# Kernel optimization log

Hardware: AMD Instinct MI355X
Metric: run time of the kernel (lower is better)

Reference implementation:

```python
import jax, jax.numpy as jnp
import numpy as np

B, N, C = 8, 2000, 81
MAX_INST = 100
MIN_CONF = 0.7
NMS_THR = 0.3
BBOX_STD = jnp.array([0.1, 0.1, 0.2, 0.2], dtype=jnp.float32)
CLASS_OFFSET = 4.0  # per-class box offset so one NMS == per-class NMS


def setup_inputs() -> dict:
    key = jax.random.key(0)
    k1, k2, k3, k4 = jax.random.split(key, 4)
    # well-formed normalized rois: y1<y2, x1<x2
    ctr = jax.random.uniform(k1, (B, N, 2), minval=0.2, maxval=0.8)
    sz = jax.random.uniform(k2, (B, N, 2), minval=0.02, maxval=0.3)
    y1x1 = jnp.clip(ctr - 0.5 * sz, 0.0, 1.0)
    y2x2 = jnp.clip(ctr + 0.5 * sz, 0.0, 1.0)
    rois = jnp.concatenate([y1x1, y2x2], axis=-1).astype(jnp.float32)
    mrcnn_class = jax.nn.softmax(4.0 * jax.random.normal(k3, (B, N, C)), axis=-1).astype(jnp.float32)
    mrcnn_bbox = (0.1 * jax.random.normal(k4, (B, N, C, 4))).astype(jnp.float32)
    # meta: [image_id(1), orig_shape(3), image_shape(3), window(4), scale(1), active_class_ids(C)]
    meta_row = np.concatenate([
        np.array([0.0]), np.array([1024.0, 1024.0, 3.0]), np.array([1024.0, 1024.0, 3.0]),
        np.array([0.0, 0.0, 1024.0, 1024.0]), np.array([1.0]), np.ones(C)]).astype(np.float32)
    image_meta = jnp.broadcast_to(jnp.asarray(meta_row), (B, 12 + C))
    return {"rois": rois, "mrcnn_class": mrcnn_class, "mrcnn_bbox": mrcnn_bbox, "image_meta": image_meta}


def _apply_box_deltas(boxes, deltas):  # [N,4],[N,4]
    h = boxes[:, 2] - boxes[:, 0]
    w = boxes[:, 3] - boxes[:, 1]
    cy = boxes[:, 0] + 0.5 * h + deltas[:, 0] * h
    cx = boxes[:, 1] + 0.5 * w + deltas[:, 1] * w
    h = h * jnp.exp(deltas[:, 2])
    w = w * jnp.exp(deltas[:, 3])
    return jnp.stack([cy - 0.5 * h, cx - 0.5 * w, cy + 0.5 * h, cx + 0.5 * w], axis=1)


def _clip_boxes(boxes, window):  # window: [4]
    wy1, wx1, wy2, wx2 = window[0], window[1], window[2], window[3]
    y1 = jnp.clip(boxes[:, 0], wy1, wy2)
    x1 = jnp.clip(boxes[:, 1], wx1, wx2)
    y2 = jnp.clip(boxes[:, 2], wy1, wy2)
    x2 = jnp.clip(boxes[:, 3], wx1, wx2)
    return jnp.stack([y1, x1, y2, x2], axis=1)


def _pairwise_iou(b):  # [N,4] -> [N,N]
    area = (b[:, 2] - b[:, 0]) * (b[:, 3] - b[:, 1])
    iy = jnp.maximum(0.0, jnp.minimum(b[:, None, 2], b[None, :, 2]) - jnp.maximum(b[:, None, 0], b[None, :, 0]))
    ix = jnp.maximum(0.0, jnp.minimum(b[:, None, 3], b[None, :, 3]) - jnp.maximum(b[:, None, 1], b[None, :, 1]))
    inter = iy * ix
    return inter / (area[:, None] + area[None, :] - inter + 1e-12)


def _refine_one(rois, probs, deltas, window):
    n = rois.shape[0]
    class_ids = jnp.argmax(probs, axis=1)                      # [N]
    idx = jnp.arange(n)
    scores = probs[idx, class_ids]                              # [N]
    ds = deltas[idx, class_ids] * BBOX_STD                      # [N,4]
    refined = _clip_boxes(_apply_box_deltas(rois, ds), window)  # [N,4]
    valid = (class_ids > 0) & (scores >= MIN_CONF)
    # per-class NMS via class-offset trick (classes can never overlap)
    off_boxes = refined + CLASS_OFFSET * class_ids.astype(jnp.float32)[:, None]
    order = jnp.argsort(-jnp.where(valid, scores, -1.0))
    b_sorted = off_boxes[order]
    iou = _pairwise_iou(b_sorted)                               # [N,N]
    pos = jnp.arange(n)

    def body(keep, i):
        sup = keep[i] & (iou[i] > NMS_THR) & (pos > i)
        return keep & ~sup, None

    keep_sorted, _ = jax.lax.scan(body, valid[order], pos)
    keep = jnp.zeros(n, bool).at[order].set(keep_sorted)
    # per-class cap at MAX_INST (mirror max_output_size of per-class NMS)
    same = class_ids[:, None] == class_ids[None, :]
    before = (scores[None, :] > scores[:, None]) | ((scores[None, :] == scores[:, None]) & (pos[None, :] < pos[:, None]))
    rank = jnp.sum(keep[None, :] & same & before, axis=1)
    keep = keep & (rank < MAX_INST)
    # global top-k by score, pad with zeros
    masked = jnp.where(keep, scores, -1.0)
    top_scores, top_idx = jax.lax.top_k(masked, MAX_INST)
    valid_out = top_scores > 0.0
    det = jnp.concatenate([
        refined[top_idx],
        class_ids[top_idx].astype(jnp.float32)[:, None],
        scores[top_idx][:, None]], axis=1)                      # [MAX_INST,6]
    return jnp.where(valid_out[:, None], det, 0.0)


def reference(rois, mrcnn_class, mrcnn_bbox, image_meta):
    # normalize per-image window using image_shape of first image (as in original)
    image_shape = image_meta[0, 4:7]
    h, w = image_shape[0], image_shape[1]
    scale = jnp.stack([h, w, h, w]) - 1.0
    shift = jnp.array([0.0, 0.0, 1.0, 1.0], dtype=jnp.float32)
    window = (image_meta[:, 7:11] - shift) / scale              # [B,4]
    det = jax.vmap(_refine_one)(rois, mrcnn_class, mrcnn_bbox, window)
    return det.reshape(rois.shape[0], MAX_INST, 6)
```

## Files before the change

### kernel.cpp

```cpp
#include <hip/hip_runtime.h>
#include <stdint.h>

#define Bn 8
#define Nn 2000
#define Cc 81
#define META_STRIDE (12 + Cc)
#define MAXI 100
#define MINCONF 0.7f
#define NMSTHR 0.3f
#define PB_ROIS 128
#define PSTRIDE 83
#define SELT 320
#define SELCAP 512

__device__ __forceinline__ uint32_t ford(float f) {
    uint32_t u = __float_as_uint(f);
    return (u & 0x80000000u) ? ~u : (u | 0x80000000u);
}

__device__ __forceinline__ unsigned long long shflx64(unsigned long long v, int lx) {
    unsigned int lo = (unsigned int)v, hi = (unsigned int)(v >> 32);
    lo = (unsigned int)__shfl_xor((int)lo, lx, 64);
    hi = (unsigned int)__shfl_xor((int)hi, lx, 64);
    return ((unsigned long long)hi << 32) | lo;
}

__global__ void __launch_bounds__(256)
k_prep(const float* __restrict__ rois,
       const float* __restrict__ probs,
       const float* __restrict__ bbox,
       const float* __restrict__ meta,
       float* __restrict__ refined,
       float* __restrict__ score,
       int* __restrict__ cls,
       unsigned long long* __restrict__ keys) {
    __shared__ float sp[PB_ROIS * PSTRIDE];
    int tid  = threadIdx.x;
    int base = blockIdx.x * PB_ROIS;

    const float* gp = probs + (size_t)base * Cc;
    const int total = PB_ROIS * Cc;
    int r = tid / Cc, c = tid - r * Cc;
    for (int idx = tid; idx < total; idx += 256) {
        sp[r * PSTRIDE + c] = gp[idx];
        r += 3; c += 13;
        if (c >= Cc) { c -= Cc; r += 1; }
    }
    __syncthreads();

    int row  = tid >> 1;
    int half = tid & 1;
    const float* sr = sp + row * PSTRIDE;
    int   c0 = half ? 41 : 0;
    int   c1 = half ? Cc : 41;
    float v  = sr[c0];
    int   cb = c0;
    for (int cc2 = c0 + 1; cc2 < c1; ++cc2) {
        float x = sr[cc2];
        if (x > v) { v = x; cb = cc2; }
    }
    float vo = __shfl_xor(v, 1, 64);
    int   co = __shfl_xor(cb, 1, 64);
    float vA = half ? vo : v;   int cA = half ? co : cb;
    float vB = half ? v  : vo;  int cB = half ? cb : co;
    float sbest;  int cbest;
    if (vB > vA) { sbest = vB; cbest = cB; }
    else         { sbest = vA; cbest = cA; }

    if (half) return;
    int t = base + row;

    float4 d4 = reinterpret_cast<const float4*>(bbox)[(size_t)t * Cc + cbest];
    float dy = d4.x * 0.1f, dx = d4.y * 0.1f, dh = d4.z * 0.2f, dw = d4.w * 0.2f;

    float4 r4 = reinterpret_cast<const float4*>(rois)[t];
    float y1 = r4.x, x1 = r4.y, y2 = r4.z, x2 = r4.w;
    float h = y2 - y1, w = x2 - x1;
    float cy = y1 + 0.5f * h + dy * h;
    float cx = x1 + 0.5f * w + dx * w;
    h = h * expf(dh);
    w = w * expf(dw);
    float ny1 = cy - 0.5f * h, nx1 = cx - 0.5f * w;
    float ny2 = cy + 0.5f * h, nx2 = cx + 0.5f * w;

    int b = t / Nn;
    float sy = meta[4] - 1.0f, sx = meta[5] - 1.0f;
    const float* mb = meta + (size_t)b * META_STRIDE;
    float wy1 = mb[7] / sy;
    float wx1 = mb[8] / sx;
    float wy2 = (mb[9]  - 1.0f) / sy;
    float wx2 = (mb[10] - 1.0f) / sx;

    ny1 = fminf(fmaxf(ny1, wy1), wy2);
    nx1 = fminf(fmaxf(nx1, wx1), wx2);
    ny2 = fminf(fmaxf(ny2, wy1), wy2);
    nx2 = fminf(fmaxf(nx2, wx1), wx2);

    reinterpret_cast<float4*>(refined)[t] = float4{ny1, nx1, ny2, nx2};
    score[t] = sbest;
    cls[t]   = cbest;

    int i = t - b * Nn;
    bool valid = (cbest > 0) && (sbest >= MINCONF);
    float ks = valid ? sbest : -1.0f;
    keys[t] = ((unsigned long long)ford(ks) << 32) |
              (unsigned long long)(0xFFFFFFFFu - (uint32_t)i);
}

__global__ void __launch_bounds__(1024, 1)
k_select(const unsigned long long* __restrict__ keys,
         unsigned long long* __restrict__ selk,
         int* __restrict__ selcnt) {
    __shared__ int h1[256], h2[256], sc[256];
    __shared__ int sB, sSuf, sTheta, scnt;

    int b = blockIdx.x, tid = threadIdx.x;
    const unsigned long long* kb = keys + (size_t)b * Nn;
    int e0 = tid << 1;
    unsigned long long k0 = (e0     < Nn) ? kb[e0]     : 0ull;
    unsigned long long k1 = (e0 + 1 < Nn) ? kb[e0 + 1] : 0ull;

    if (tid < 256) { h1[tid] = 0; h2[tid] = 0; }
    if (tid == 0) { sB = -2; sSuf = 0; sTheta = 0x8000; scnt = 0; }
    __syncthreads();

    if (k0 >> 63) atomicAdd(&h1[(int)(k0 >> 56) & 255], 1);
    if (k1 >> 63) atomicAdd(&h1[(int)(k1 >> 56) & 255], 1);
    __syncthreads();

    if (tid < 256) sc[tid] = h1[tid];
    __syncthreads();
    for (int off = 1; off < 256; off <<= 1) {
        int v = 0;
        if (tid < 256 && tid + off < 256) v = sc[tid + off];
        __syncthreads();
        if (tid < 256) sc[tid] += v;
        __syncthreads();
    }
    if (tid < 256) {
        int c  = sc[tid];
        int cn = (tid < 255) ? sc[tid + 1] : 0;
        if (c >= SELT && cn < SELT) { sB = tid; sSuf = cn; }
    }
    __syncthreads();
    int B = sB;

    if (B >= 0) {
        if ((k0 >> 63) && (((int)(k0 >> 56) & 255) == B))
            atomicAdd(&h2[(int)(k0 >> 48) & 255], 1);
        if ((k1 >> 63) && (((int)(k1 >> 56) & 255) == B))
            atomicAdd(&h2[(int)(k1 >> 48) & 255], 1);
        __syncthreads();
        if (tid < 256) sc[tid] = h2[tid];
        __syncthreads();
        for (int off = 1; off < 256; off <<= 1) {
            int v = 0;
            if (tid < 256 && tid + off < 256) v = sc[tid + off];
            __syncthreads();
            if (tid < 256) sc[tid] += v;
            __syncthreads();
        }
        if (tid < 256) {
            int c  = sSuf + sc[tid];
            int cn = sSuf + ((tid < 255) ? sc[tid + 1] : 0);
            if (c >= SELT && cn < SELT) sTheta = (B << 8) | tid;
        }
    }
    __syncthreads();

    unsigned th = (unsigned)sTheta;
    if ((unsigned)(k0 >> 48) >= th) {
        int s = atomicAdd(&scnt, 1);
        if (s < SELCAP) selk[b * SELCAP + s] = k0;
    }
    if ((unsigned)(k1 >> 48) >= th) {
        int s = atomicAdd(&scnt, 1);
        if (s < SELCAP) selk[b * SELCAP + s] = k1;
    }
    __syncthreads();
    if (tid == 0) { int c = scnt; selcnt[b] = c < SELCAP ? c : SELCAP; }
}

__global__ void __launch_bounds__(1024, 1)
k_rest(const unsigned long long* __restrict__ selk,
       const int* __restrict__ selcnt,
       const float* __restrict__ refined,
       const float* __restrict__ score,
       const int* __restrict__ cls,
       float* __restrict__ out) {
    __shared__ unsigned long long sk[SELCAP];
    __shared__ float4 sboxL[SELCAP];
    __shared__ unsigned long long intraw[64];
    __shared__ unsigned long long extw[16];
    __shared__ int klist[128];
    __shared__ int sNk;

    int b = blockIdx.x, tid = threadIdx.x;
    int wid = tid >> 6, lane = tid & 63;
    int e0 = tid << 1;

    int S = selcnt[b];
    if (tid < SELCAP) sk[tid] = (tid < S) ? selk[b * SELCAP + tid] : 0ull;
    if (tid == 0) sNk = 0;
    __syncthreads();

    if (tid < 256) {
        unsigned long long a = sk[e0], bv = sk[e0 + 1];
        for (int k = 2; k <= 128; k <<= 1) {
            bool desc = ((e0 & k) == 0);
            for (int j = k >> 1; j >= 2; j >>= 1) {
                int lx = j >> 1;
                bool keepmax = (desc == ((lane & lx) == 0));
                unsigned long long oa = shflx64(a, lx);
                unsigned long long ob = shflx64(bv, lx);
                a  = keepmax ? (a  > oa ? a  : oa) : (a  < oa ? a  : oa);
                bv = keepmax ? (bv > ob ? bv : ob) : (bv < ob ? bv : ob);
            }
            bool sw = desc ? (a < bv) : (a > bv);
            if (sw) { unsigned long long t2 = a; a = bv; bv = t2; }
        }
        sk[e0] = a; sk[e0 + 1] = bv;
    }
    __syncthreads();

    for (int k = 256; k <= SELCAP; k <<= 1) {
        for (int j = k >> 1; j >= 128; j >>= 1) {
            for (int t = tid; t < SELCAP; t += 1024) {
                int ixj = t ^ j;
                if (ixj > t) {
                    unsigned long long x = sk[t], y = sk[ixj];
                    bool desc = ((t & k) == 0);
                    if (desc ? (x < y) : (x > y)) { sk[t] = y; sk[ixj] = x; }
                }
            }
            __syncthreads();
        }
        if (tid < 256) {
            unsigned long long a = sk[e0], bv = sk[e0 + 1];
            bool desc = ((e0 & k) == 0);
            #pragma unroll
            for (int lx = 32; lx >= 1; lx >>= 1) {
                bool keepmax = (desc == ((lane & lx) == 0));
                unsigned long long oa = shflx64(a, lx);
                unsigned long long ob = shflx64(bv, lx);
                a  = keepmax ? (a  > oa ? a  : oa) : (a  < oa ? a  : oa);
                bv = keepmax ? (bv > ob ? bv : ob) : (bv < ob ? bv : ob);
            }
            bool sw = desc ? (a < bv) : (a > bv);
            if (sw) { unsigned long long t2 = a; a = bv; bv = t2; }
            sk[e0] = a; sk[e0 + 1] = bv;
        }
        __syncthreads();
    }

    for (int t = tid; t < S; t += 1024) {
        uint32_t oi = 0xFFFFFFFFu - (uint32_t)(sk[t] & 0xFFFFFFFFull);
        int gi = b * Nn + (int)oi;
        float off = 4.0f * (float)cls[gi];
        float4 rf = reinterpret_cast<const float4*>(refined)[gi];
        sboxL[t] = float4{rf.x + off, rf.y + off, rf.z + off, rf.w + off};
    }
    __syncthreads();

    int nblocks = (S + 63) >> 6;
    for (int t = 0; t < nblocks; ++t) {
        int base = t << 6;
        int nb = S - base; if (nb > 64) nb = 64;
        int K = sNk;

        float4 cb = (lane < nb) ? sboxL[base + lane] : float4{0.f, 0.f, 0.f, 0.f};
        float a2 = (cb.z - cb.x) * (cb.w - cb.y);

        bool supext = false;
        for (int k = wid; k < K; k += 16) {
            float4 kbx = sboxL[klist[k]];
            float ar = (kbx.z - kbx.x) * (kbx.w - kbx.y);
            float iy = fmaxf(0.0f, fminf(kbx.z, cb.z) - fmaxf(kbx.x, cb.x));
            float ix = fmaxf(0.0f, fminf(kbx.w, cb.w) - fmaxf(kbx.y, cb.y));
            float inter = iy * ix;
            float iou = inter / (ar + a2 - inter + 1e-12f);
            supext |= (lane < nb) && (iou > NMSTHR);
        }
        unsigned long long bw = __ballot(supext);
        if (lane == 0) extw[wid] = bw;

        #pragma unroll
        for (int s = 0; s < 4; ++s) {
            int rr = (wid << 2) + s;
            bool sup = false;
            if (rr < nb && lane < nb && lane > rr) {
                float4 rb = sboxL[base + rr];
                float ar = (rb.z - rb.x) * (rb.w - rb.y);
                float iy = fmaxf(0.0f, fminf(rb.z, cb.z) - fmaxf(rb.x, cb.x));
                float ix = fmaxf(0.0f, fminf(rb.w, cb.w) - fmaxf(rb.y, cb.y));
                float inter = iy * ix;
                float iou = inter / (ar + a2 - inter + 1e-12f);
                sup = iou > NMSTHR;
            }
            unsigned long long rb2 = __ballot(sup);
            if (lane == 0) intraw[rr] = rb2;
        }
        __syncthreads();

        if (wid == 0) {
            unsigned long long intra_l = intraw[lane];
            unsigned long long e = (lane < 16) ? extw[lane] : 0ull;
            #pragma unroll
            for (int m = 8; m >= 1; m >>= 1) e |= __shfl_xor(e, m, 64);
            e = __shfl(e, 0, 64);

            int nk = K;
            bool alive = (lane < nb) && !((e >> lane) & 1ull);
            unsigned long long candm = __ballot(alive);
            while (candm) {
                int i = __builtin_ctzll(candm);
                if (lane == 0) klist[nk] = base + i;
                ++nk;
                if (nk >= MAXI) break;
                unsigned long long rowi = __shfl(intra_l, i, 64);
                alive = alive && !((rowi >> lane) & 1ull);
                candm = __ballot(alive) & ~((2ull << i) - 1ull);
            }
            if (lane == 0) sNk = nk;
        }
        __syncthreads();
        if (sNk >= MAXI) break;
    }

    int ne = sNk < MAXI ? sNk : MAXI;
    for (int r = tid; r < ne; r += 1024) {
        int pos = klist[r];
        uint32_t oi = 0xFFFFFFFFu - (uint32_t)(sk[pos] & 0xFFFFFFFFull);
        int gi = b * Nn + (int)oi;
        float4 rf = reinterpret_cast<const float4*>(refined)[gi];
        float* orow = out + ((size_t)b * MAXI + r) * 6;
        orow[0] = rf.x;
        orow[1] = rf.y;
        orow[2] = rf.z;
        orow[3] = rf.w;
        orow[4] = (float)cls[gi];
        orow[5] = score[gi];
    }
    for (int tt = ne * 6 + tid; tt < MAXI * 6; tt += 1024)
        out[(size_t)b * MAXI * 6 + tt] = 0.0f;
}

extern "C" void kernel_launch(void* const* d_in, const int* in_sizes, int n_in,
                              void* d_out, int out_size, void* d_ws, size_t ws_size,
                              hipStream_t stream) {
    const float* rois  = (const float*)d_in[0];
    const float* probs = (const float*)d_in[1];
    const float* bbox  = (const float*)d_in[2];
    const float* meta  = (const float*)d_in[3];
    float* out = (float*)d_out;

    const int BN = Bn * Nn;
    char* ws = (char*)d_ws;
    size_t off = 0;
    auto alloc = [&](size_t bytes) {
        void* p = ws + off;
        off += (bytes + 255) & ~(size_t)255;
        return p;
    };
    float*              refined = (float*)              alloc((size_t)BN * 4 * sizeof(float));
    float*              score   = (float*)              alloc((size_t)BN * sizeof(float));
    int*                cls     = (int*)                alloc((size_t)BN * sizeof(int));
    unsigned long long* keys    = (unsigned long long*) alloc((size_t)BN * sizeof(unsigned long long));
    unsigned long long* selk    = (unsigned long long*) alloc((size_t)Bn * SELCAP * sizeof(unsigned long long));
    int*                selcnt  = (int*)                alloc((size_t)Bn * sizeof(int));
    (void)ws_size; (void)in_sizes; (void)n_in; (void)out_size;

    k_prep<<<BN / PB_ROIS, 256, 0, stream>>>(rois, probs, bbox, meta,
                                             refined, score, cls, keys);
    k_select<<<Bn, 1024, 0, stream>>>(keys, selk, selcnt);
    k_rest<<<Bn, 1024, 0, stream>>>(selk, selcnt, refined, score, cls, out);
}
```

Measured before the change: 40.90 us.

## Fuse candidate selection into NMS kernel and use wave-shuffle histogram scans

Merges the top-candidate selection kernel into the NMS/output kernel so that selected keys go straight into shared memory. This removes one kernel launch and the global round trip for the selected keys and their count. It also replaces the 256-entry Hillis-Steele suffix scan, which needed a barrier at every step, with a single-wavefront scan: each lane sums four bins, then the lanes combine with shuffles. Only one wave does the scan work, so the rest of the block idles during that phase.

New measurement: 38.06 us, median of 2. 1.07x faster.

```diff
diff --git a/kernel.cpp b/kernel.cpp
--- a/kernel.cpp
+++ b/kernel.cpp
@@ -108,38 +108,52 @@
 }
 
 __global__ void __launch_bounds__(1024, 1)
-k_select(const unsigned long long* __restrict__ keys,
-         unsigned long long* __restrict__ selk,
-         int* __restrict__ selcnt) {
-    __shared__ int h1[256], h2[256], sc[256];
-    __shared__ int sB, sSuf, sTheta, scnt;
+k_nms(const unsigned long long* __restrict__ keys,
+      const float* __restrict__ refined,
+      const float* __restrict__ score,
+      const int* __restrict__ cls,
+      float* __restrict__ out) {
+    __shared__ unsigned long long sk[SELCAP];
+    __shared__ float4 sboxL[SELCAP];
+    __shared__ int h1[256], h2[256], sc[257];
+    __shared__ unsigned long long intraw[64];
+    __shared__ unsigned long long extw[16];
+    __shared__ int klist[128];
+    __shared__ int sNk, sB, sSuf, sTheta, scnt;
 
     int b = blockIdx.x, tid = threadIdx.x;
+    int wid = tid >> 6, lane = tid & 63;
+    int e0 = tid << 1;
+
     const unsigned long long* kb = keys + (size_t)b * Nn;
-    int e0 = tid << 1;
     unsigned long long k0 = (e0     < Nn) ? kb[e0]     : 0ull;
     unsigned long long k1 = (e0 + 1 < Nn) ? kb[e0 + 1] : 0ull;
 
     if (tid < 256) { h1[tid] = 0; h2[tid] = 0; }
-    if (tid == 0) { sB = -2; sSuf = 0; sTheta = 0x8000; scnt = 0; }
+    if (tid < SELCAP) sk[tid] = 0ull;
+    if (tid == 0) { sB = -2; sSuf = 0; sTheta = 0x8000; scnt = 0; sNk = 0; sc[256] = 0; }
     __syncthreads();
 
     if (k0 >> 63) atomicAdd(&h1[(int)(k0 >> 56) & 255], 1);
     if (k1 >> 63) atomicAdd(&h1[(int)(k1 >> 56) & 255], 1);
     __syncthreads();
 
-    if (tid < 256) sc[tid] = h1[tid];
-    __syncthreads();
-    for (int off = 1; off < 256; off <<= 1) {
-        int v = 0;
-        if (tid < 256 && tid + off < 256) v = sc[tid + off];
-        __syncthreads();
-        if (tid < 256) sc[tid] += v;
-        __syncthreads();
-    }
+    if (wid == 0) {
+        int b0 = lane << 2;
+        int v0 = h1[b0], v1 = h1[b0 + 1], v2 = h1[b0 + 2], v3 = h1[b0 + 3];
+        int s3 = v3, s2 = v2 + s3, s1 = v1 + s2, s0 = v0 + s1;
+        int G = s0;
+        #pragma unroll
+        for (int off = 1; off < 64; off <<= 1) {
+            int u = __shfl_down(G, off, 64);
+            if (lane + off < 64) G += u;
+        }
+        int A = G - s0;
+        sc[b0] = A + s0; sc[b0 + 1] = A + s1; sc[b0 + 2] = A + s2; sc[b0 + 3] = A + s3;
+    }
+    __syncthreads();
     if (tid < 256) {
-        int c  = sc[tid];
-        int cn = (tid < 255) ? sc[tid + 1] : 0;
+        int c = sc[tid], cn = sc[tid + 1];
         if (c >= SELT && cn < SELT) { sB = tid; sSuf = cn; }
     }
     __syncthreads();
@@ -151,18 +165,23 @@
         if ((k1 >> 63) && (((int)(k1 >> 56) & 255) == B))
             atomicAdd(&h2[(int)(k1 >> 48) & 255], 1);
         __syncthreads();
-        if (tid < 256) sc[tid] = h2[tid];
-        __syncthreads();
-        for (int off = 1; off < 256; off <<= 1) {
-            int v = 0;
-            if (tid < 256 && tid + off < 256) v = sc[tid + off];
-            __syncthreads();
-            if (tid < 256) sc[tid] += v;
-            __syncthreads();
-        }
+        if (wid == 0) {
+            int b0 = lane << 2;
+            int v0 = h2[b0], v1 = h2[b0 + 1], v2 = h2[b0 + 2], v3 = h2[b0 + 3];
+            int s3 = v3, s2 = v2 + s3, s1 = v1 + s2, s0 = v0 + s1;
+            int G = s0;
+            #pragma unroll
+            for (int off = 1; off < 64; off <<= 1) {
+                int u = __shfl_down(G, off, 64);
+                if (lane + off < 64) G += u;
+            }
+            int A = G - s0;
+            sc[b0] = A + s0; sc[b0 + 1] = A + s1; sc[b0 + 2] = A + s2; sc[b0 + 3] = A + s3;
+        }
+        __syncthreads();
         if (tid < 256) {
             int c  = sSuf + sc[tid];
-            int cn = sSuf + ((tid < 255) ? sc[tid + 1] : 0);
+            int cn = sSuf + sc[tid + 1];
             if (c >= SELT && cn < SELT) sTheta = (B << 8) | tid;
         }
     }
@@ -171,38 +190,14 @@
     unsigned th = (unsigned)sTheta;
     if ((unsigned)(k0 >> 48) >= th) {
         int s = atomicAdd(&scnt, 1);
-        if (s < SELCAP) selk[b * SELCAP + s] = k0;
+        if (s < SELCAP) sk[s] = k0;
     }
     if ((unsigned)(k1 >> 48) >= th) {
         int s = atomicAdd(&scnt, 1);
-        if (s < SELCAP) selk[b * SELCAP + s] = k1;
-    }
-    __syncthreads();
-    if (tid == 0) { int c = scnt; selcnt[b] = c < SELCAP ? c : SELCAP; }
-}
-
-__global__ void __launch_bounds__(1024, 1)
-k_rest(const unsigned long long* __restrict__ selk,
-       const int* __restrict__ selcnt,
-       const float* __restrict__ refined,
-       const float* __restrict__ score,
-       const int* __restrict__ cls,
-       float* __restrict__ out) {
-    __shared__ unsigned long long sk[SELCAP];
-    __shared__ float4 sboxL[SELCAP];
-    __shared__ unsigned long long intraw[64];
-    __shared__ unsigned long long extw[16];
-    __shared__ int klist[128];
-    __shared__ int sNk;
-
-    int b = blockIdx.x, tid = threadIdx.x;
-    int wid = tid >> 6, lane = tid & 63;
-    int e0 = tid << 1;
-
-    int S = selcnt[b];
-    if (tid < SELCAP) sk[tid] = (tid < S) ? selk[b * SELCAP + tid] : 0ull;
-    if (tid == 0) sNk = 0;
-    __syncthreads();
+        if (s < SELCAP) sk[s] = k1;
+    }
+    __syncthreads();
+    int S = scnt; if (S > SELCAP) S = SELCAP;
 
     if (tid < 256) {
         unsigned long long a = sk[e0], bv = sk[e0 + 1];
@@ -366,12 +361,9 @@
     float*              score   = (float*)              alloc((size_t)BN * sizeof(float));
     int*                cls     = (int*)                alloc((size_t)BN * sizeof(int));
     unsigned long long* keys    = (unsigned long long*) alloc((size_t)BN * sizeof(unsigned long long));
-    unsigned long long* selk    = (unsigned long long*) alloc((size_t)Bn * SELCAP * sizeof(unsigned long long));
-    int*                selcnt  = (int*)                alloc((size_t)Bn * sizeof(int));
     (void)ws_size; (void)in_sizes; (void)n_in; (void)out_size;
 
     k_prep<<<BN / PB_ROIS, 256, 0, stream>>>(rois, probs, bbox, meta,
                                              refined, score, cls, keys);
-    k_select<<<Bn, 1024, 0, stream>>>(keys, selk, selcnt);
-    k_rest<<<Bn, 1024, 0, stream>>>(selk, selcnt, refined, score, cls, out);
-}
+    k_nms<<<Bn, 1024, 0, stream>>>(keys, refined, score, cls, out);
+}
```
